# Optimization experiments

Measured on AMD Instinct MI355X. Metric: run time of the kernel, lower is better.

The kernel has to match this reference:

```python
import jax, jax.numpy as jnp
import numpy as np

N_NODES = 50000
N_EDGES = 400000
IN_CH = 7
EMBED = 128
EDGE_DIM = 6


def setup_inputs() -> dict:
    key = jax.random.key(0)
    ks = jax.random.split(key, 10)
    x = jax.random.normal(ks[0], (N_NODES, IN_CH), dtype=jnp.float32)
    edge_index = jax.random.randint(ks[1], (2, N_EDGES), 0, N_NODES, dtype=jnp.int64)
    edge_attr = jax.random.normal(ks[2], (N_EDGES, EDGE_DIM), dtype=jnp.float32)
    # edge MLP params: Linear(6,128) -> GELU -> Linear(128, 7*128)
    s1 = 1.0 / np.sqrt(EDGE_DIM)
    s2 = 1.0 / np.sqrt(EMBED)
    W1 = jax.random.uniform(ks[3], (EDGE_DIM, EMBED), jnp.float32, -s1, s1)
    b1 = jax.random.uniform(ks[4], (EMBED,), jnp.float32, -s1, s1)
    W2 = jax.random.uniform(ks[5], (EMBED, IN_CH * EMBED), jnp.float32, -s2, s2)
    b2 = jax.random.uniform(ks[6], (IN_CH * EMBED,), jnp.float32, -s2, s2)
    # NNConv root weight and bias
    s3 = 1.0 / np.sqrt(IN_CH)
    root = jax.random.uniform(ks[7], (IN_CH, EMBED), jnp.float32, -s3, s3)
    bias = jnp.zeros((EMBED,), dtype=jnp.float32)
    return {"x": x, "edge_index": edge_index, "edge_attr": edge_attr,
            "W1": W1, "b1": b1, "W2": W2, "b2": b2, "root": root, "bias": bias}


def reference(x, edge_index, edge_attr, W1, b1, W2, b2, root, bias):
    N = x.shape[0]
    src, dst = edge_index[0], edge_index[1]
    # edge MLP -> per-edge weight matrix [E, in_ch, embed]
    h = jax.nn.gelu(edge_attr @ W1 + b1, approximate=False)
    w = (h @ W2 + b2).reshape(-1, IN_CH, EMBED)
    # gather source node features, per-edge small matmul
    msg = jnp.einsum('ei,eio->eo', x[src], w)  # [E, embed]
    # mean aggregation at target nodes
    summed = jax.ops.segment_sum(msg, dst, num_segments=N)
    cnt = jax.ops.segment_sum(jnp.ones((msg.shape[0],), msg.dtype), dst, num_segments=N)
    aggr = summed / jnp.clip(cnt, 1.0)[:, None]
    return aggr + x @ root + bias
```

## Files before the change

kernel.cpp:

```cpp
#include <hip/hip_runtime.h>
#include <stdint.h>

#define NNODES 50000
#define NEDGES 400000
#define INCH 7
#define EMB 128
#define EDIM 6
#define KD 896
#define BM 128
#define NSTEPS 28

typedef __attribute__((ext_vector_type(8))) short bf16x8;
typedef __attribute__((ext_vector_type(4))) float f32x4;

__device__ __forceinline__ short f2bf(float f) {
  union { float f; uint32_t u; } v; v.f = f;
  uint32_t r = v.u + 0x7FFFu + ((v.u >> 16) & 1u);
  return (short)(r >> 16);
}

__device__ __forceinline__ float fast_gelu(float x) {
  float x2 = x * x;
  float y = x * (0.7978845608f + 0.03567740814f * x2);
  float e = __expf(2.0f * y);
  float t = 1.0f - 2.0f / (1.0f + e);
  return 0.5f * x * (1.0f + t);
}

__global__ void prep_B(const float* __restrict__ W2, short* __restrict__ Bp) {
  int idx = blockIdx.x * 256 + threadIdx.x;
  int m    = idx & 7;
  int r    = (idx >> 3) & 15;
  int kseg = (idx >> 7) & 3;
  int nh   = (idx >> 9) & 7;
  int step = idx >> 12;
  int i = step >> 2, kk = step & 3;
  int k = kk * 32 + kseg * 8 + m;
  int o = nh * 16 + r;
  Bp[idx] = f2bf(W2[k * KD + i * EMB + o]);
}

__global__ __launch_bounds__(256, 2)
void nnconv_main(const float* __restrict__ x,
                 const int* __restrict__ ei,
                 const float* __restrict__ ea,
                 const float* __restrict__ W1,
                 const float* __restrict__ b1,
                 const float* __restrict__ b2,
                 const short* __restrict__ Bp,
                 float* __restrict__ cnt,
                 float* __restrict__ out) {
  __shared__ __align__(16) short h_s[BM * EMB];
  __shared__ __align__(16) float x_s[BM][9];
  __shared__ __align__(16) float ea_s[BM * EDIM];
  __shared__ __align__(16) float w1_s[EDIM * EMB];
  __shared__ __align__(16) float b1_s[EMB];
  __shared__ __align__(16) float b2_s[KD];
  __shared__ int dst_s[BM];

  const int t = threadIdx.x;
  const int lane = t & 63;
  const int w = t >> 6;
  const int eb = blockIdx.x * BM;

  if (t < 192) {
    *(float4*)&ea_s[t * 4] = *(const float4*)&ea[(size_t)eb * EDIM + t * 4];
    *(float4*)&w1_s[t * 4] = *(const float4*)&W1[t * 4];
  }
  if (t >= 192 && t < 224) { int q = t - 192; *(float4*)&b1_s[q * 4] = *(const float4*)&b1[q * 4]; }
  if (t < 224) *(float4*)&b2_s[t * 4] = *(const float4*)&b2[t * 4];
  if (t < BM) {
    int s = ei[eb + t];
    int d = ei[NEDGES + eb + t];
    dst_s[t] = d;
#pragma unroll
    for (int i = 0; i < 7; ++i) x_s[t][i] = x[s * 7 + i];
    atomicAdd(&cnt[d], 1.0f);
  }
  __syncthreads();

  {
    const int e = t >> 1, half = t & 1;
    float a[6];
#pragma unroll
    for (int q = 0; q < 6; ++q) a[q] = ea_s[e * 6 + q];
    const int swz = (e & 15) << 4;
#pragma unroll
    for (int j = 0; j < 8; ++j) {
      bf16x8 hv;
#pragma unroll
      for (int m = 0; m < 8; ++m) {
        int c = half * 64 + j * 8 + m;
        float pre = b1_s[c];
#pragma unroll
        for (int q = 0; q < 6; ++q) pre += a[q] * w1_s[q * EMB + c];
        hv[m] = f2bf(fast_gelu(pre));
      }
      int addr = e * 256 + ((half * 128 + j * 16) ^ swz);
      *(bf16x8*)((char*)h_s + addr) = hv;
    }
  }
  __syncthreads();

  const int wm = w >> 1, wn = w & 1;
  const int rowA = lane & 15;
  const int kseg = lane >> 4;
  const char* BpByte = (const char*)Bp + (size_t)lane * 16;

  f32x4 acc[4][4];
#pragma unroll
  for (int fm = 0; fm < 4; ++fm)
#pragma unroll
    for (int fn = 0; fn < 4; ++fn) acc[fm][fn] = f32x4{0.f, 0.f, 0.f, 0.f};

  bf16x8 bcur[4], bnxt[4];
#pragma unroll
  for (int fn = 0; fn < 4; ++fn)
    bcur[fn] = *(const bf16x8*)(BpByte + ((0 * 8 + wn * 4 + fn) << 10));

#pragma unroll 1
  for (int i = 0; i < 7; ++i) {
    f32x4 tmp[4][4];
#pragma unroll
    for (int fm = 0; fm < 4; ++fm)
#pragma unroll
      for (int fn = 0; fn < 4; ++fn) tmp[fm][fn] = f32x4{0.f, 0.f, 0.f, 0.f};

#pragma unroll
    for (int kk = 0; kk < 4; ++kk) {
      const int step = i * 4 + kk;
      if (step < NSTEPS - 1) {
#pragma unroll
        for (int fn = 0; fn < 4; ++fn)
          bnxt[fn] = *(const bf16x8*)(BpByte + (((step + 1) * 8 + wn * 4 + fn) << 10));
      }
      bf16x8 af[4];
#pragma unroll
      for (int fm = 0; fm < 4; ++fm) {
        int row = wm * 64 + fm * 16 + rowA;
        int col = (kk * 64 + kseg * 16) ^ ((row & 15) << 4);
        af[fm] = *(const bf16x8*)((const char*)h_s + row * 256 + col);
      }
#pragma unroll
      for (int fm = 0; fm < 4; ++fm)
#pragma unroll
        for (int fn = 0; fn < 4; ++fn)
          tmp[fm][fn] = __builtin_amdgcn_mfma_f32_16x16x32_bf16(af[fm], bcur[fn], tmp[fm][fn], 0, 0, 0);
#pragma unroll
      for (int fn = 0; fn < 4; ++fn) bcur[fn] = bnxt[fn];
    }
#pragma unroll
    for (int fm = 0; fm < 4; ++fm) {
#pragma unroll
      for (int r = 0; r < 4; ++r) {
        float xv = x_s[wm * 64 + fm * 16 + kseg * 4 + r][i];
#pragma unroll
        for (int fn = 0; fn < 4; ++fn) acc[fm][fn][r] += xv * tmp[fm][fn][r];
      }
    }
  }

  const int colA = rowA;
  float bb[4][7];
#pragma unroll
  for (int fn = 0; fn < 4; ++fn)
#pragma unroll
    for (int i = 0; i < 7; ++i) bb[fn][i] = b2_s[i * EMB + wn * 64 + fn * 16 + colA];

#pragma unroll
  for (int fm = 0; fm < 4; ++fm) {
#pragma unroll
    for (int r = 0; r < 4; ++r) {
      const int row = wm * 64 + fm * 16 + kseg * 4 + r;
      float xr[7];
#pragma unroll
      for (int i = 0; i < 7; ++i) xr[i] = x_s[row][i];
      const int d = dst_s[row];
      float* op = out + (size_t)d * EMB + wn * 64 + colA;
#pragma unroll
      for (int fn = 0; fn < 4; ++fn) {
        float v = acc[fm][fn][r];
#pragma unroll
        for (int i = 0; i < 7; ++i) v += xr[i] * bb[fn][i];
        atomicAdd(op + fn * 16, v);
      }
    }
  }
}

__global__ void finalize(const float* __restrict__ x, const float* __restrict__ root,
                         const float* __restrict__ bias, const float* __restrict__ cnt,
                         float* __restrict__ out) {
  int idx = blockIdx.x * 256 + threadIdx.x;
  int n = idx >> 7, o = idx & 127;
  float c = fmaxf(cnt[n], 1.0f);
  float v = out[idx] / c + bias[o];
#pragma unroll
  for (int i = 0; i < 7; ++i) v += x[n * 7 + i] * root[i * EMB + o];
  out[idx] = v;
}

extern "C" void kernel_launch(void* const* d_in, const int* in_sizes, int n_in,
                              void* d_out, int out_size, void* d_ws, size_t ws_size,
                              hipStream_t stream) {
  const float* x    = (const float*)d_in[0];
  const int*   ei   = (const int*)d_in[1];
  const float* ea   = (const float*)d_in[2];
  const float* W1   = (const float*)d_in[3];
  const float* b1   = (const float*)d_in[4];
  const float* W2   = (const float*)d_in[5];
  const float* b2   = (const float*)d_in[6];
  const float* root = (const float*)d_in[7];
  const float* bias = (const float*)d_in[8];
  float* out = (float*)d_out;

  short* Bp  = (short*)d_ws;
  float* cnt = (float*)((char*)d_ws + 128 * KD * 2);

  hipMemsetAsync(out, 0, (size_t)NNODES * EMB * sizeof(float), stream);
  hipMemsetAsync(cnt, 0, (size_t)NNODES * sizeof(float), stream);
  prep_B<<<448, 256, 0, stream>>>(W2, Bp);
  nnconv_main<<<NEDGES / BM, 256, 0, stream>>>(x, ei, ea, W1, b1, b2, Bp, cnt, out);
  finalize<<<NNODES * EMB / 256, 256, 0, stream>>>(x, root, bias, cnt, out);
}
```

Measured before the change: 313.1 us.

## Compute first edge-MLP layer with split-bf16 MFMA and restructure B prefetch

The first layer (edge_attr @ W1 + b1) now runs on MFMA, with W1 and edge_attr split into hi/lo bf16 parts packed into the K dimension to keep near-fp32 accuracy. A new prep_W1 kernel packs W1. This replaces the scalar per-thread FMA loop and drops the W1, b1 and b2 shared-memory staging. The main GEMM is reorganised into half-N passes with a 4-deep register ring of B fragments prefetched two steps ahead. The GELU is simplified to use a hardware reciprocal, and launch bounds rise to 3 blocks per SM. This cuts register pressure and ALU work, at the cost of scalar LDS stores of h and some precision risk.

```diff
diff --git a/kernel.cpp b/kernel.cpp
--- a/kernel.cpp
+++ b/kernel.cpp
@@ -3,12 +3,9 @@
 
 #define NNODES 50000
 #define NEDGES 400000
-#define INCH 7
 #define EMB 128
-#define EDIM 6
 #define KD 896
 #define BM 128
-#define NSTEPS 28
 
 typedef __attribute__((ext_vector_type(8))) short bf16x8;
 typedef __attribute__((ext_vector_type(4))) float f32x4;
@@ -18,57 +15,74 @@
   uint32_t r = v.u + 0x7FFFu + ((v.u >> 16) & 1u);
   return (short)(r >> 16);
 }
-
+__device__ __forceinline__ float bf2f(short s) {
+  union { uint32_t u; float f; } v; v.u = ((uint32_t)(uint16_t)s) << 16;
+  return v.f;
+}
 __device__ __forceinline__ float fast_gelu(float x) {
   float x2 = x * x;
   float y = x * (0.7978845608f + 0.03567740814f * x2);
   float e = __expf(2.0f * y);
-  float t = 1.0f - 2.0f / (1.0f + e);
-  return 0.5f * x * (1.0f + t);
+  float r = __builtin_amdgcn_rcpf(1.0f + e);
+  return x - x * r;
 }
 
 __global__ void prep_B(const float* __restrict__ W2, short* __restrict__ Bp) {
   int idx = blockIdx.x * 256 + threadIdx.x;
-  int m    = idx & 7;
-  int r    = (idx >> 3) & 15;
-  int kseg = (idx >> 7) & 3;
-  int nh   = (idx >> 9) & 7;
-  int step = idx >> 12;
-  int i = step >> 2, kk = step & 3;
-  int k = kk * 32 + kseg * 8 + m;
-  int o = nh * 16 + r;
+  int m = idx & 7, l = (idx >> 3) & 63, c = idx >> 9;
+  int sidx = c >> 2, wn = (c >> 1) & 1, f = c & 1;
+  int p = sidx >> 2, kk = sidx & 3, i = p >> 1, fnh = p & 1;
+  int o = (wn * 4 + fnh * 2 + f) * 16 + (l & 15);
+  int k = kk * 32 + (l >> 4) * 8 + m;
   Bp[idx] = f2bf(W2[k * KD + i * EMB + o]);
 }
 
-__global__ __launch_bounds__(256, 2)
+__global__ void prep_W1(const float* __restrict__ W1f, short* __restrict__ W1p) {
+  int idx = blockIdx.x * 256 + threadIdx.x;
+  int m = idx & 7, lane = (idx >> 3) & 63, nf = idx >> 9;
+  int col = nf * 16 + (lane & 15), kseg = lane >> 4;
+  short outv = 0;
+  if (m < 6 && kseg < 3) {
+    float wv = W1f[m * EMB + col];
+    short hi = f2bf(wv);
+    outv = (kseg == 2) ? f2bf(wv - bf2f(hi)) : hi;
+  }
+  W1p[idx] = outv;
+}
+
+__global__ __launch_bounds__(256, 3)
 void nnconv_main(const float* __restrict__ x,
                  const int* __restrict__ ei,
                  const float* __restrict__ ea,
-                 const float* __restrict__ W1,
                  const float* __restrict__ b1,
                  const float* __restrict__ b2,
                  const short* __restrict__ Bp,
+                 const short* __restrict__ W1p,
                  float* __restrict__ cnt,
                  float* __restrict__ out) {
   __shared__ __align__(16) short h_s[BM * EMB];
   __shared__ __align__(16) float x_s[BM][9];
-  __shared__ __align__(16) float ea_s[BM * EDIM];
-  __shared__ __align__(16) float w1_s[EDIM * EMB];
-  __shared__ __align__(16) float b1_s[EMB];
-  __shared__ __align__(16) float b2_s[KD];
+  __shared__ __align__(16) float ea_s[BM * 6];
   __shared__ int dst_s[BM];
 
   const int t = threadIdx.x;
   const int lane = t & 63;
   const int w = t >> 6;
+  const int wm = w >> 1, wn = w & 1;
+  const int rowA = lane & 15;
+  const int kseg = lane >> 4;
   const int eb = blockIdx.x * BM;
 
-  if (t < 192) {
-    *(float4*)&ea_s[t * 4] = *(const float4*)&ea[(size_t)eb * EDIM + t * 4];
-    *(float4*)&w1_s[t * 4] = *(const float4*)&W1[t * 4];
-  }
-  if (t >= 192 && t < 224) { int q = t - 192; *(float4*)&b1_s[q * 4] = *(const float4*)&b1[q * 4]; }
-  if (t < 224) *(float4*)&b2_s[t * 4] = *(const float4*)&b2[t * 4];
+  const char* BpB = (const char*)Bp + lane * 16 + wn * 2048;
+  bf16x8 bfr[4][2];
+#pragma unroll
+  for (int s = 0; s < 4; ++s)
+#pragma unroll
+    for (int f = 0; f < 2; ++f)
+      bfr[s][f] = *(const bf16x8*)(BpB + (((size_t)s * 4 + f) << 10));
+
+  if (t < 192)
+    *(float4*)&ea_s[t * 4] = *(const float4*)&ea[(size_t)eb * 6 + t * 4];
   if (t < BM) {
     int s = ei[eb + t];
     int d = ei[NEDGES + eb + t];
@@ -80,95 +94,114 @@
   __syncthreads();
 
   {
-    const int e = t >> 1, half = t & 1;
-    float a[6];
-#pragma unroll
-    for (int q = 0; q < 6; ++q) a[q] = ea_s[e * 6 + q];
-    const int swz = (e & 15) << 4;
-#pragma unroll
-    for (int j = 0; j < 8; ++j) {
-      bf16x8 hv;
-#pragma unroll
-      for (int m = 0; m < 8; ++m) {
-        int c = half * 64 + j * 8 + m;
-        float pre = b1_s[c];
-#pragma unroll
-        for (int q = 0; q < 6; ++q) pre += a[q] * w1_s[q * EMB + c];
-        hv[m] = f2bf(fast_gelu(pre));
-      }
-      int addr = e * 256 + ((half * 128 + j * 16) ^ swz);
-      *(bf16x8*)((char*)h_s + addr) = hv;
+    bf16x8 aef[2];
+#pragma unroll
+    for (int fm2 = 0; fm2 < 2; ++fm2) {
+      int re = w * 32 + fm2 * 16 + rowA;
+      bf16x8 av = (bf16x8){0, 0, 0, 0, 0, 0, 0, 0};
+#pragma unroll
+      for (int q = 0; q < 6; ++q) {
+        float eq = ea_s[re * 6 + q];
+        short hq = f2bf(eq);
+        short lq = f2bf(eq - bf2f(hq));
+        short v = (kseg == 1) ? lq : hq;
+        av[q] = (kseg == 3) ? (short)0 : v;
+      }
+      aef[fm2] = av;
+    }
+#pragma unroll
+    for (int half = 0; half < 2; ++half) {
+      bf16x8 wf[4];
+      f32x4 cf[2][4];
+#pragma unroll
+      for (int j = 0; j < 4; ++j)
+        wf[j] = *(const bf16x8*)(W1p + ((half * 4 + j) * 64 + lane) * 8);
+#pragma unroll
+      for (int j = 0; j < 4; ++j) {
+        float bc = b1[(half * 4 + j) * 16 + rowA];
+        f32x4 ci = (f32x4){bc, bc, bc, bc};
+#pragma unroll
+        for (int fm2 = 0; fm2 < 2; ++fm2)
+          cf[fm2][j] = __builtin_amdgcn_mfma_f32_16x16x32_bf16(aef[fm2], wf[j], ci, 0, 0, 0);
+      }
+#pragma unroll
+      for (int fm2 = 0; fm2 < 2; ++fm2)
+#pragma unroll
+        for (int j = 0; j < 4; ++j)
+#pragma unroll
+          for (int r = 0; r < 4; ++r) {
+            int row = w * 32 + fm2 * 16 + kseg * 4 + r;
+            int col = (half * 4 + j) * 16 + rowA;
+            short hv = f2bf(fast_gelu(cf[fm2][j][r]));
+            *(short*)((char*)h_s + row * 256 + ((col * 2) ^ ((row & 15) << 4))) = hv;
+          }
     }
   }
   __syncthreads();
 
-  const int wm = w >> 1, wn = w & 1;
-  const int rowA = lane & 15;
-  const int kseg = lane >> 4;
-  const char* BpByte = (const char*)Bp + (size_t)lane * 16;
-
   f32x4 acc[4][4];
 #pragma unroll
-  for (int fm = 0; fm < 4; ++fm)
-#pragma unroll
-    for (int fn = 0; fn < 4; ++fn) acc[fm][fn] = f32x4{0.f, 0.f, 0.f, 0.f};
-
-  bf16x8 bcur[4], bnxt[4];
-#pragma unroll
-  for (int fn = 0; fn < 4; ++fn)
-    bcur[fn] = *(const bf16x8*)(BpByte + ((0 * 8 + wn * 4 + fn) << 10));
+  for (int a = 0; a < 4; ++a)
+#pragma unroll
+    for (int b = 0; b < 4; ++b) acc[a][b] = (f32x4){0.f, 0.f, 0.f, 0.f};
 
 #pragma unroll 1
   for (int i = 0; i < 7; ++i) {
-    f32x4 tmp[4][4];
-#pragma unroll
-    for (int fm = 0; fm < 4; ++fm)
-#pragma unroll
-      for (int fn = 0; fn < 4; ++fn) tmp[fm][fn] = f32x4{0.f, 0.f, 0.f, 0.f};
-
-#pragma unroll
-    for (int kk = 0; kk < 4; ++kk) {
-      const int step = i * 4 + kk;
-      if (step < NSTEPS - 1) {
-#pragma unroll
-        for (int fn = 0; fn < 4; ++fn)
-          bnxt[fn] = *(const bf16x8*)(BpByte + (((step + 1) * 8 + wn * 4 + fn) << 10));
-      }
-      bf16x8 af[4];
-#pragma unroll
-      for (int fm = 0; fm < 4; ++fm) {
-        int row = wm * 64 + fm * 16 + rowA;
-        int col = (kk * 64 + kseg * 16) ^ ((row & 15) << 4);
-        af[fm] = *(const bf16x8*)((const char*)h_s + row * 256 + col);
+#pragma unroll
+    for (int fnh = 0; fnh < 2; ++fnh) {
+      const int p = i * 2 + fnh;
+      const int s0 = p * 4;
+      f32x4 tmp[4][2];
+#pragma unroll
+      for (int a = 0; a < 4; ++a) {
+        tmp[a][0] = (f32x4){0.f, 0.f, 0.f, 0.f};
+        tmp[a][1] = (f32x4){0.f, 0.f, 0.f, 0.f};
+      }
+#pragma unroll
+      for (int kk = 0; kk < 4; ++kk) {
+        bf16x8 af[4];
+#pragma unroll
+        for (int fm = 0; fm < 4; ++fm) {
+          int row = wm * 64 + fm * 16 + rowA;
+          int col = (kk * 64 + kseg * 16) ^ ((row & 15) << 4);
+          af[fm] = *(const bf16x8*)((const char*)h_s + row * 256 + col);
+        }
+#pragma unroll
+        for (int fm = 0; fm < 4; ++fm) {
+          tmp[fm][0] = __builtin_amdgcn_mfma_f32_16x16x32_bf16(af[fm], bfr[kk][0], tmp[fm][0], 0, 0, 0);
+          tmp[fm][1] = __builtin_amdgcn_mfma_f32_16x16x32_bf16(af[fm], bfr[kk][1], tmp[fm][1], 0, 0, 0);
+        }
+        if ((kk == 1 || kk == 3) && p < 13) {
+          const int sn = s0 + 4 + ((kk == 3) ? 2 : 0);
+          const int slot = (kk == 1) ? 0 : 2;
+#pragma unroll
+          for (int u = 0; u < 2; ++u)
+#pragma unroll
+            for (int f = 0; f < 2; ++f)
+              bfr[slot + u][f] = *(const bf16x8*)(BpB + (((size_t)(sn + u) * 4 + f) << 10));
+        }
       }
 #pragma unroll
       for (int fm = 0; fm < 4; ++fm)
 #pragma unroll
-        for (int fn = 0; fn < 4; ++fn)
-          tmp[fm][fn] = __builtin_amdgcn_mfma_f32_16x16x32_bf16(af[fm], bcur[fn], tmp[fm][fn], 0, 0, 0);
-#pragma unroll
-      for (int fn = 0; fn < 4; ++fn) bcur[fn] = bnxt[fn];
-    }
-#pragma unroll
-    for (int fm = 0; fm < 4; ++fm) {
-#pragma unroll
-      for (int r = 0; r < 4; ++r) {
-        float xv = x_s[wm * 64 + fm * 16 + kseg * 4 + r][i];
-#pragma unroll
-        for (int fn = 0; fn < 4; ++fn) acc[fm][fn][r] += xv * tmp[fm][fn][r];
-      }
+        for (int r = 0; r < 4; ++r) {
+          float xv = x_s[wm * 64 + fm * 16 + kseg * 4 + r][i];
+          acc[fm][fnh * 2 + 0][r] += xv * tmp[fm][0][r];
+          acc[fm][fnh * 2 + 1][r] += xv * tmp[fm][1][r];
+        }
     }
   }
 
   const int colA = rowA;
   float bb[4][7];
 #pragma unroll
-  for (int fn = 0; fn < 4; ++fn)
-#pragma unroll
-    for (int i = 0; i < 7; ++i) bb[fn][i] = b2_s[i * EMB + wn * 64 + fn * 16 + colA];
-
-#pragma unroll
-  for (int fm = 0; fm < 4; ++fm) {
+  for (int j = 0; j < 4; ++j)
+#pragma unroll
+    for (int i = 0; i < 7; ++i)
+      bb[j][i] = b2[i * EMB + wn * 64 + j * 16 + colA];
+
+#pragma unroll
+  for (int fm = 0; fm < 4; ++fm)
 #pragma unroll
     for (int r = 0; r < 4; ++r) {
       const int row = wm * 64 + fm * 16 + kseg * 4 + r;
@@ -178,14 +211,13 @@
       const int d = dst_s[row];
       float* op = out + (size_t)d * EMB + wn * 64 + colA;
 #pragma unroll
-      for (int fn = 0; fn < 4; ++fn) {
-        float v = acc[fm][fn][r];
-#pragma unroll
-        for (int i = 0; i < 7; ++i) v += xr[i] * bb[fn][i];
-        atomicAdd(op + fn * 16, v);
-      }
-    }
-  }
+      for (int j = 0; j < 4; ++j) {
+        float v = acc[fm][j][r];
+#pragma unroll
+        for (int i = 0; i < 7; ++i) v += xr[i] * bb[j][i];
+        atomicAdd(op + j * 16, v);
+      }
+    }
 }
 
 __global__ void finalize(const float* __restrict__ x, const float* __restrict__ root,
@@ -215,11 +247,13 @@
   float* out = (float*)d_out;
 
   short* Bp  = (short*)d_ws;
-  float* cnt = (float*)((char*)d_ws + 128 * KD * 2);
+  short* W1p = (short*)((char*)d_ws + 128 * KD * 2);
+  float* cnt = (float*)((char*)d_ws + 128 * KD * 2 + 8192);
 
   hipMemsetAsync(out, 0, (size_t)NNODES * EMB * sizeof(float), stream);
   hipMemsetAsync(cnt, 0, (size_t)NNODES * sizeof(float), stream);
   prep_B<<<448, 256, 0, stream>>>(W2, Bp);
-  nnconv_main<<<NEDGES / BM, 256, 0, stream>>>(x, ei, ea, W1, b1, b2, Bp, cnt, out);
+  prep_W1<<<16, 256, 0, stream>>>(W1, W1p);
+  nnconv_main<<<NEDGES / BM, 256, 0, stream>>>(x, ei, ea, b1, b2, Bp, W1p, cnt, out);
   finalize<<<NNODES * EMB / 256, 256, 0, stream>>>(x, root, bias, cnt, out);
 }
```

New measurement: 862.9 us. 176% more time.
